# Optimization experiments

Hardware: AMD Instinct MI355X
Metric: run time of the kernel (lower is better)

The kernel has to match this reference:

```python
import jax, jax.numpy as jnp
import numpy as np

N_NODES = 50000
N_EDGES = 800000
NUM_FEATURES = 128
HIDDEN = 128
EMBED = 64
OUT_DIM = 1


def setup_inputs() -> dict:
    key = jax.random.key(0)
    ks = jax.random.split(key, 12)
    x = jax.random.normal(ks[0], (N_NODES, NUM_FEATURES), dtype=jnp.float32)
    edge_index = jax.random.randint(ks[1], (2, N_EDGES), 0, N_NODES, dtype=jnp.int64)

    def glorot(k, fan_in, fan_out):
        s = jnp.sqrt(6.0 / (fan_in + fan_out)).astype(jnp.float32)
        return jax.random.uniform(k, (fan_in, fan_out), jnp.float32, -s, s)

    return {
        "x": x,
        "edge_index": edge_index,
        "W1": glorot(ks[2], NUM_FEATURES, HIDDEN),
        "b1": jnp.zeros((HIDDEN,), jnp.float32),
        "Wh": glorot(ks[3], HIDDEN, HIDDEN),
        "bh": jnp.zeros((HIDDEN,), jnp.float32),
        "W2": glorot(ks[4], HIDDEN, EMBED),
        "b2": jnp.zeros((EMBED,), jnp.float32),
        "Wout": glorot(ks[5], EMBED, OUT_DIM),
        "bout": jnp.zeros((OUT_DIM,), jnp.float32),
    }


def _gcn_norm(edge_index, num_nodes):
    # Add self-loops, compute symmetric normalization deg^{-1/2} A_hat deg^{-1/2}
    loop = jnp.arange(num_nodes, dtype=edge_index.dtype)
    src = jnp.concatenate([edge_index[0], loop])
    dst = jnp.concatenate([edge_index[1], loop])
    deg = jax.ops.segment_sum(jnp.ones_like(dst, dtype=jnp.float32), dst,
                              num_segments=num_nodes)
    dis = jnp.where(deg > 0, jax.lax.rsqrt(jnp.maximum(deg, 1.0)), 0.0)
    norm = dis[src] * dis[dst]  # [E+N]
    return src, dst, norm


def _gcn_conv(h, W, b, src, dst, norm, num_nodes):
    h = h @ W  # linear transform first (PyG GCNConv)
    msg = h[src] * norm[:, None]  # gather + scale
    return jax.ops.segment_sum(msg, dst, num_segments=num_nodes) + b


def reference(x, edge_index, W1, b1, Wh, bh, W2, b2, Wout, bout):
    n = x.shape[0]
    src, dst, norm = _gcn_norm(edge_index, n)
    h = jax.nn.relu(_gcn_conv(x, W1, b1, src, dst, norm, n))  # dropout p=0 -> identity
    h = jax.nn.relu(_gcn_conv(h, Wh, bh, src, dst, norm, n))
    h = _gcn_conv(h, W2, b2, src, dst, norm, n)
    out = h @ Wout + bout
    return (out, h)
```

## Files before the change

kernel.cpp:

```cpp
#include <hip/hip_runtime.h>
#include <hip/hip_bf16.h>


#define N_NODES 50000
#define N_EDGES 800000
#define NBUCK 196
#define GB 196
#define EPB 4096

typedef __attribute__((ext_vector_type(8))) short short8;
typedef __attribute__((ext_vector_type(8))) unsigned short ushort8v;
typedef __attribute__((ext_vector_type(4))) float f32x4;

static __device__ __forceinline__ unsigned short f2bf(float f) {
    __hip_bfloat16 h = __float2bfloat16(f);
    return *reinterpret_cast<unsigned short*>(&h);
}
static __device__ __forceinline__ float bf2f(unsigned short u) {
    return __uint_as_float(((unsigned)u) << 16);
}

__global__ __launch_bounds__(256) void hist_wprep_kernel(
    const int* __restrict__ dstv, int* __restrict__ H, int nE, int* __restrict__ ticket,
    const float* __restrict__ W1, const float* __restrict__ Wh, const float* __restrict__ W2,
    unsigned short* __restrict__ W1hi, unsigned short* __restrict__ W1lo,
    unsigned short* __restrict__ Whhi, unsigned short* __restrict__ Whlo,
    unsigned short* __restrict__ W2hi, unsigned short* __restrict__ W2lo) {
    int gt = blockIdx.x * 256 + threadIdx.x;
    if (gt == 0) *ticket = 0;
    if (gt < 40960) {
        const float* W; unsigned short *Hi, *Lo; int nout, lt;
        if (gt < 16384)      { W = W1; Hi = W1hi; Lo = W1lo; nout = 128; lt = gt; }
        else if (gt < 32768) { W = Wh; Hi = Whhi; Lo = Whlo; nout = 128; lt = gt - 16384; }
        else                 { W = W2; Hi = W2hi; Lo = W2lo; nout = 64;  lt = gt - 32768; }
        int col = lt % nout, k = lt / nout;
        float v = W[lt];
        unsigned short hi = f2bf(v);
        unsigned short lo = f2bf(v - bf2f(hi));
        Hi[(size_t)col * 128 + k] = hi;
        Lo[(size_t)col * 128 + k] = lo;
    }

    __shared__ int h[NBUCK];
    for (int i = threadIdx.x; i < NBUCK; i += 256) h[i] = 0;
    __syncthreads();
    int base = blockIdx.x * EPB;
#pragma unroll
    for (int i = 0; i < EPB / 256; ++i) {
        int e = base + i * 256 + threadIdx.x;
        if (e < nE) atomicAdd(&h[dstv[e] >> 8], 1);
    }
    __syncthreads();
    for (int i = threadIdx.x; i < NBUCK; i += 256)
        H[i * GB + blockIdx.x] = h[i];
}

__global__ __launch_bounds__(256) void scan_kernel(int* __restrict__ H,
                                                   int* __restrict__ bsum,
                                                   int* __restrict__ bstart,
                                                   int* __restrict__ rowoff_last,
                                                   int* __restrict__ ticket) {
    __shared__ int s[256];
    __shared__ int lastFlag;
    int t = threadIdx.x, k = blockIdx.x;
    int v = (t < GB) ? H[k * GB + t] : 0;
    s[t] = v;
    __syncthreads();
    for (int off = 1; off < 256; off <<= 1) {
        int u = (t >= off) ? s[t - off] : 0;
        __syncthreads();
        s[t] += u;
        __syncthreads();
    }
    if (t < GB) H[k * GB + t] = s[t] - v;
    if (t == 255) {
        bsum[k] = s[255];
        __threadfence();
        int tk = atomicAdd(ticket, 1);
        lastFlag = (tk == NBUCK - 1);
    }
    __syncthreads();
    if (!lastFlag) return;
    __threadfence();
    int v2 = (t < NBUCK) ? bsum[t] : 0;
    s[t] = v2;
    __syncthreads();
    for (int off = 1; off < 256; off <<= 1) {
        int u = (t >= off) ? s[t - off] : 0;
        __syncthreads();
        s[t] += u;
        __syncthreads();
    }
    if (t < NBUCK) bstart[t] = s[t] - v2;
    if (t == 0) { bstart[NBUCK] = N_EDGES; *rowoff_last = N_EDGES; }
}

__global__ __launch_bounds__(256) void partition_kernel(const int* __restrict__ srcv,
                                                        const int* __restrict__ dstv,
                                                        const int* __restrict__ H,
                                                        const int* __restrict__ bstart,
                                                        unsigned int* __restrict__ P, int nE) {
    __shared__ int cur[NBUCK];
    for (int i = threadIdx.x; i < NBUCK; i += 256)
        cur[i] = bstart[i] + H[i * GB + blockIdx.x];
    __syncthreads();
    int base = blockIdx.x * EPB;
#pragma unroll
    for (int i = 0; i < EPB / 256; ++i) {
        int e = base + i * 256 + threadIdx.x;
        if (e < nE) {
            int d = dstv[e];
            unsigned int pk = (unsigned int)srcv[e] | ((unsigned int)(d & 255) << 16);
            int pos = atomicAdd(&cur[d >> 8], 1);
            P[pos] = pk;
        }
    }
}

__global__ __launch_bounds__(256) void bucket_csr_kernel(const unsigned int* __restrict__ P,
                                                         const int* __restrict__ bstart,
                                                         int* __restrict__ rowoff,
                                                         float* __restrict__ dis,
                                                         unsigned short* __restrict__ csr_src, int n) {
    __shared__ int cnt[256];
    __shared__ int s[256];
    __shared__ int cur[256];
    int t = threadIdx.x, k = blockIdx.x;
    int ebeg = bstart[k], eend = bstart[k + 1];
    cnt[t] = 0;
    __syncthreads();
    for (int e = ebeg + t; e < eend; e += 256)
        atomicAdd(&cnt[(P[e] >> 16) & 255], 1);
    __syncthreads();
    int myc = cnt[t];
    s[t] = myc;
    __syncthreads();
    for (int off = 1; off < 256; off <<= 1) {
        int v = (t >= off) ? s[t - off] : 0;
        __syncthreads();
        s[t] += v;
        __syncthreads();
    }
    int excl = s[t] - myc;
    int node = (k << 8) + t;
    if (node < n) {
        rowoff[node] = ebeg + excl;
        dis[node] = rsqrtf((float)(myc + 1));
    }
    cur[t] = ebeg + excl;
    __syncthreads();
    for (int e = ebeg + t; e < eend; e += 256) {
        unsigned int p = P[e];
        int pos = atomicAdd(&cur[(p >> 16) & 255], 1);
        csr_src[pos] = (unsigned short)(p & 0xFFFFu);
    }
}

template <int NOUT, bool SPLITA>
__global__ __launch_bounds__(256) void gemm_mfma_kernel(
    const float* __restrict__ A,
    const unsigned short* __restrict__ Ahi, const unsigned short* __restrict__ Alo,
    const unsigned short* __restrict__ Wthi, const unsigned short* __restrict__ Wtlo,
    const float* __restrict__ scale, unsigned short* __restrict__ C, int M) {
    constexpr int LDK = 136;
    __shared__ unsigned short sAhi[64 * LDK];
    __shared__ unsigned short sAlo[64 * LDK];

    int tid = threadIdx.x;
    int w = tid >> 6, lane = tid & 63;
    int quad = lane >> 4, m = lane & 15;
    int Rbase = blockIdx.x * 64, Cbase = blockIdx.y * 64;
    int r0 = (w & 1) * 32, c0 = (w >> 1) * 32;

    short8 bh[4][2], bl[4][2];
#pragma unroll
    for (int ks = 0; ks < 4; ++ks)
#pragma unroll
        for (int g = 0; g < 2; ++g) {
            size_t off = (size_t)(Cbase + c0 + g * 16 + m) * 128 + ks * 32 + quad * 8;
            bh[ks][g] = *(const short8*)(Wthi + off);
            bl[ks][g] = *(const short8*)(Wtlo + off);
        }

    if constexpr (SPLITA) {
        for (int i = tid; i < 64 * 16; i += 256) {
            int r = i >> 4, c8 = i & 15;
            int row = Rbase + r;
            short8 hv = {0,0,0,0,0,0,0,0}, lv = {0,0,0,0,0,0,0,0};
            if (row < M) {
                hv = *(const short8*)(Ahi + (size_t)row * 128 + c8 * 8);
                lv = *(const short8*)(Alo + (size_t)row * 128 + c8 * 8);
            }
            *(short8*)(sAhi + r * LDK + c8 * 8) = hv;
            *(short8*)(sAlo + r * LDK + c8 * 8) = lv;
        }
    } else {
        for (int i = tid; i < 64 * 32; i += 256) {
            int r = i >> 5, c4 = i & 31;
            int row = Rbase + r;
            float4 v = make_float4(0.f, 0.f, 0.f, 0.f);
            if (row < M) v = ((const float4*)(A + (size_t)row * 128))[c4];
            ushort4 hi, lo;
            hi.x = f2bf(v.x); lo.x = f2bf(v.x - bf2f(hi.x));
            hi.y = f2bf(v.y); lo.y = f2bf(v.y - bf2f(hi.y));
            hi.z = f2bf(v.z); lo.z = f2bf(v.z - bf2f(hi.z));
            hi.w = f2bf(v.w); lo.w = f2bf(v.w - bf2f(hi.w));
            *(ushort4*)(sAhi + r * LDK + c4 * 4) = hi;
            *(ushort4*)(sAlo + r * LDK + c4 * 4) = lo;
        }
    }
    __syncthreads();

    f32x4 z = {0.f, 0.f, 0.f, 0.f};
    f32x4 acc00 = z, acc01 = z, acc10 = z, acc11 = z;

#pragma unroll
    for (int ks = 0; ks < 4; ++ks) {
        int kof = ks * 32 + quad * 8;
        short8 ah0 = *(const short8*)(sAhi + (r0 + m) * LDK + kof);
        short8 ah1 = *(const short8*)(sAhi + (r0 + 16 + m) * LDK + kof);
        short8 al0 = *(const short8*)(sAlo + (r0 + m) * LDK + kof);
        short8 al1 = *(const short8*)(sAlo + (r0 + 16 + m) * LDK + kof);
        acc00 = __builtin_amdgcn_mfma_f32_16x16x32_bf16(ah0, bh[ks][0], acc00, 0, 0, 0);
        acc01 = __builtin_amdgcn_mfma_f32_16x16x32_bf16(ah0, bh[ks][1], acc01, 0, 0, 0);
        acc10 = __builtin_amdgcn_mfma_f32_16x16x32_bf16(ah1, bh[ks][0], acc10, 0, 0, 0);
        acc11 = __builtin_amdgcn_mfma_f32_16x16x32_bf16(ah1, bh[ks][1], acc11, 0, 0, 0);
        acc00 = __builtin_amdgcn_mfma_f32_16x16x32_bf16(ah0, bl[ks][0], acc00, 0, 0, 0);
        acc01 = __builtin_amdgcn_mfma_f32_16x16x32_bf16(ah0, bl[ks][1], acc01, 0, 0, 0);
        acc10 = __builtin_amdgcn_mfma_f32_16x16x32_bf16(ah1, bl[ks][0], acc10, 0, 0, 0);
        acc11 = __builtin_amdgcn_mfma_f32_16x16x32_bf16(ah1, bl[ks][1], acc11, 0, 0, 0);
        acc00 = __builtin_amdgcn_mfma_f32_16x16x32_bf16(al0, bh[ks][0], acc00, 0, 0, 0);
        acc01 = __builtin_amdgcn_mfma_f32_16x16x32_bf16(al0, bh[ks][1], acc01, 0, 0, 0);
        acc10 = __builtin_amdgcn_mfma_f32_16x16x32_bf16(al1, bh[ks][0], acc10, 0, 0, 0);
        acc11 = __builtin_amdgcn_mfma_f32_16x16x32_bf16(al1, bh[ks][1], acc11, 0, 0, 0);
    }

#pragma unroll
    for (int reg = 0; reg < 4; ++reg) {
        int row0g = Rbase + r0 + quad * 4 + reg;
        if (row0g < M) {
            float sc = scale[row0g];
            C[(size_t)row0g * NOUT + Cbase + c0 + m]      = f2bf(acc00[reg] * sc);
            C[(size_t)row0g * NOUT + Cbase + c0 + 16 + m] = f2bf(acc01[reg] * sc);
        }
        int row1g = row0g + 16;
        if (row1g < M) {
            float sc = scale[row1g];
            C[(size_t)row1g * NOUT + Cbase + c0 + m]      = f2bf(acc10[reg] * sc);
            C[(size_t)row1g * NOUT + Cbase + c0 + 16 + m] = f2bf(acc11[reg] * sc);
        }
    }
}

__global__ __launch_bounds__(256) void aggregate128_kernel(
    const int* __restrict__ rowoff, const unsigned short* __restrict__ csr_src,
    const float* __restrict__ dis, const unsigned short* __restrict__ tp,
    const float* __restrict__ bias,
    unsigned short* __restrict__ outHi, unsigned short* __restrict__ outLo, int n) {
    int gt = blockIdx.x * 256 + threadIdx.x;
    int node = gt >> 4;
    if (node >= n) return;
    int lc = gt & 15;

    float a[8] = {0.f,0.f,0.f,0.f,0.f,0.f,0.f,0.f};

#define ROW128(nd) (*(const ushort8v*)(tp + (size_t)(nd) * 128 + lc * 8))
#define ACC(u) { a[0] += bf2f(u[0]); a[1] += bf2f(u[1]); a[2] += bf2f(u[2]); a[3] += bf2f(u[3]); \
                 a[4] += bf2f(u[4]); a[5] += bf2f(u[5]); a[6] += bf2f(u[6]); a[7] += bf2f(u[7]); }

    { ushort8v u = ROW128(node); ACC(u); }

    int i = rowoff[node], end = rowoff[node + 1];
    for (; i + 8 <= end; i += 8) {
        int p0 = csr_src[i],     p1 = csr_src[i + 1], p2 = csr_src[i + 2], p3 = csr_src[i + 3];
        int p4 = csr_src[i + 4], p5 = csr_src[i + 5], p6 = csr_src[i + 6], p7 = csr_src[i + 7];
        ushort8v u0 = ROW128(p0), u1 = ROW128(p1), u2 = ROW128(p2), u3 = ROW128(p3);
        ushort8v u4 = ROW128(p4), u5 = ROW128(p5), u6 = ROW128(p6), u7 = ROW128(p7);
        ACC(u0); ACC(u1); ACC(u2); ACC(u3); ACC(u4); ACC(u5); ACC(u6); ACC(u7);
    }
    if (i + 4 <= end) {
        int p0 = csr_src[i], p1 = csr_src[i + 1], p2 = csr_src[i + 2], p3 = csr_src[i + 3];
        ushort8v u0 = ROW128(p0), u1 = ROW128(p1), u2 = ROW128(p2), u3 = ROW128(p3);
        ACC(u0); ACC(u1); ACC(u2); ACC(u3);
        i += 4;
    }
    if (i + 2 <= end) {
        int p0 = csr_src[i], p1 = csr_src[i + 1];
        ushort8v u0 = ROW128(p0), u1 = ROW128(p1);
        ACC(u0); ACC(u1);
        i += 2;
    }
    if (i < end) { ushort8v u = ROW128(csr_src[i]); ACC(u); }
#undef ROW128
#undef ACC

    float dd = dis[node];
    float4 b0 = ((const float4*)bias)[lc * 2];
    float4 b1 = ((const float4*)bias)[lc * 2 + 1];
    float r[8];
    r[0] = fmaxf(a[0] * dd + b0.x, 0.f);
    r[1] = fmaxf(a[1] * dd + b0.y, 0.f);
    r[2] = fmaxf(a[2] * dd + b0.z, 0.f);
    r[3] = fmaxf(a[3] * dd + b0.w, 0.f);
    r[4] = fmaxf(a[4] * dd + b1.x, 0.f);
    r[5] = fmaxf(a[5] * dd + b1.y, 0.f);
    r[6] = fmaxf(a[6] * dd + b1.z, 0.f);
    r[7] = fmaxf(a[7] * dd + b1.w, 0.f);
    ushort8v hi, lo;
#pragma unroll
    for (int j = 0; j < 8; ++j) {
        hi[j] = f2bf(r[j]);
        lo[j] = f2bf(r[j] - bf2f(hi[j]));
    }
    *(ushort8v*)(outHi + (size_t)node * 128 + lc * 8) = hi;
    *(ushort8v*)(outLo + (size_t)node * 128 + lc * 8) = lo;
}

__global__ __launch_bounds__(256) void aggregate64_head_kernel(
    const int* __restrict__ rowoff, const unsigned short* __restrict__ csr_src,
    const float* __restrict__ dis, const unsigned short* __restrict__ tp,
    const float* __restrict__ bias, const float* __restrict__ Wout,
    const float* __restrict__ bout, float* __restrict__ hout,
    float* __restrict__ out, int n) {
    int gt = blockIdx.x * 256 + threadIdx.x;
    int node = gt >> 4;
    if (node >= n) return;
    int lc = gt & 15;

    float a[4] = {0.f,0.f,0.f,0.f};

#define ROW64(nd) (*((const ushort4*)(tp + (size_t)(nd) * 64 + lc * 4)))
#define ACC2(u) { a[0] += bf2f(u.x); a[1] += bf2f(u.y); a[2] += bf2f(u.z); a[3] += bf2f(u.w); }

    { ushort4 u = ROW64(node); ACC2(u); }

    int i = rowoff[node], end = rowoff[node + 1];
    for (; i + 8 <= end; i += 8) {
        int p0 = csr_src[i],     p1 = csr_src[i + 1], p2 = csr_src[i + 2], p3 = csr_src[i + 3];
        int p4 = csr_src[i + 4], p5 = csr_src[i + 5], p6 = csr_src[i + 6], p7 = csr_src[i + 7];
        ushort4 u0 = ROW64(p0), u1 = ROW64(p1), u2 = ROW64(p2), u3 = ROW64(p3);
        ushort4 u4 = ROW64(p4), u5 = ROW64(p5), u6 = ROW64(p6), u7 = ROW64(p7);
        ACC2(u0); ACC2(u1); ACC2(u2); ACC2(u3); ACC2(u4); ACC2(u5); ACC2(u6); ACC2(u7);
    }
    if (i + 4 <= end) {
        int p0 = csr_src[i], p1 = csr_src[i + 1], p2 = csr_src[i + 2], p3 = csr_src[i + 3];
        ushort4 u0 = ROW64(p0), u1 = ROW64(p1), u2 = ROW64(p2), u3 = ROW64(p3);
        ACC2(u0); ACC2(u1); ACC2(u2); ACC2(u3);
        i += 4;
    }
    if (i + 2 <= end) {
        int p0 = csr_src[i], p1 = csr_src[i + 1];
        ushort4 u0 = ROW64(p0), u1 = ROW64(p1);
        ACC2(u0); ACC2(u1);
        i += 2;
    }
    if (i < end) { ushort4 u = ROW64(csr_src[i]); ACC2(u); }
#undef ROW64
#undef ACC2

    float dd = dis[node];
    float4 b = ((const float4*)bias)[lc];
    float4 hv;
    hv.x = a[0] * dd + b.x;
    hv.y = a[1] * dd + b.y;
    hv.z = a[2] * dd + b.z;
    hv.w = a[3] * dd + b.w;
    ((float4*)(hout + (size_t)node * 64))[lc] = hv;

    float4 wv = ((const float4*)Wout)[lc];
    float p = hv.x * wv.x + hv.y * wv.y + hv.z * wv.z + hv.w * wv.w;
#pragma unroll
    for (int off = 8; off > 0; off >>= 1) p += __shfl_xor(p, off);
    if (lc == 0) out[node] = p + bout[0];
}

extern "C" void kernel_launch(void* const* d_in, const int* in_sizes, int n_in,
                              void* d_out, int out_size, void* d_ws, size_t ws_size,
                              hipStream_t stream) {
    const float* x    = (const float*)d_in[0];
    const int*   ei   = (const int*)d_in[1];
    const float* W1   = (const float*)d_in[2];
    const float* b1   = (const float*)d_in[3];
    const float* Wh   = (const float*)d_in[4];
    const float* bh   = (const float*)d_in[5];
    const float* W2   = (const float*)d_in[6];
    const float* b2   = (const float*)d_in[7];
    const float* Wout = (const float*)d_in[8];
    const float* bout = (const float*)d_in[9];

    const int N = N_NODES;
    const int E = N_EDGES;
    const int* srcv = ei;
    const int* dstv = ei + E;

    float* out  = (float*)d_out;
    float* hout = (float*)d_out + N;

    char* ws = (char*)d_ws;
    auto alloc = [&](size_t bytes) -> char* {
        char* p = ws;
        ws += (bytes + 255) & ~(size_t)255;
        return p;
    };
    int*   H       = (int*)alloc(sizeof(int) * NBUCK * GB);
    int*   bsum    = (int*)alloc(sizeof(int) * NBUCK);
    int*   bstart  = (int*)alloc(sizeof(int) * (NBUCK + 1));
    int*   ticket  = (int*)alloc(sizeof(int) * 4);
    int*   rowoff  = (int*)alloc(sizeof(int) * (N + 1));
    unsigned int* P = (unsigned int*)alloc(sizeof(unsigned int) * E);
    unsigned short* csr_src = (unsigned short*)alloc(sizeof(unsigned short) * (E + 8));
    float* dis     = (float*)alloc(sizeof(float) * N);
    unsigned short* W1thi = (unsigned short*)alloc(sizeof(unsigned short) * 128 * 128);
    unsigned short* W1tlo = (unsigned short*)alloc(sizeof(unsigned short) * 128 * 128);
    unsigned short* Whthi = (unsigned short*)alloc(sizeof(unsigned short) * 128 * 128);
    unsigned short* Whtlo = (unsigned short*)alloc(sizeof(unsigned short) * 128 * 128);
    unsigned short* W2thi = (unsigned short*)alloc(sizeof(unsigned short) * 64 * 128);
    unsigned short* W2tlo = (unsigned short*)alloc(sizeof(unsigned short) * 64 * 128);
    unsigned short* bufT  = (unsigned short*)alloc(sizeof(unsigned short) * (size_t)N * 128);
    unsigned short* bufHi = (unsigned short*)alloc(sizeof(unsigned short) * (size_t)N * 128);
    unsigned short* bufLo = (unsigned short*)alloc(sizeof(unsigned short) * (size_t)N * 128);

    hist_wprep_kernel<<<GB, 256, 0, stream>>>(dstv, H, E, ticket,
                                              W1, Wh, W2, W1thi, W1tlo, Whthi, Whtlo, W2thi, W2tlo);
    scan_kernel<<<NBUCK, 256, 0, stream>>>(H, bsum, bstart, rowoff + N, ticket);
    partition_kernel<<<GB, 256, 0, stream>>>(srcv, dstv, H, bstart, P, E);
    bucket_csr_kernel<<<NBUCK, 256, 0, stream>>>(P, bstart, rowoff, dis, csr_src, N);

    const int aggBlocks = (N * 16 + 255) / 256;
    const int gemmRows = (N + 63) / 64;

    gemm_mfma_kernel<128, false><<<dim3(gemmRows, 2), 256, 0, stream>>>(
        x, nullptr, nullptr, W1thi, W1tlo, dis, bufT, N);
    aggregate128_kernel<<<aggBlocks, 256, 0, stream>>>(
        rowoff, csr_src, dis, bufT, b1, bufHi, bufLo, N);

    gemm_mfma_kernel<128, true><<<dim3(gemmRows, 2), 256, 0, stream>>>(
        nullptr, bufHi, bufLo, Whthi, Whtlo, dis, bufT, N);
    aggregate128_kernel<<<aggBlocks, 256, 0, stream>>>(
        rowoff, csr_src, dis, bufT, bh, bufHi, bufLo, N);

    gemm_mfma_kernel<64, true><<<dim3(gemmRows, 1), 256, 0, stream>>>(
        nullptr, bufHi, bufLo, W2thi, W2tlo, dis, bufT, N);
    aggregate64_head_kernel<<<aggBlocks, 256, 0, stream>>>(
        rowoff, csr_src, dis, bufT, b2, Wout, bout, hout, out, N);
}
```

Baseline: 258.9 us.

## Fuse aggregation with following GEMM via LDS tile and merge column blocks

```diff
diff --git a/kernel.cpp b/kernel.cpp
--- a/kernel.cpp
+++ b/kernel.cpp
@@ -156,164 +156,170 @@
     }
 }
 
-template <int NOUT, bool SPLITA>
-__global__ __launch_bounds__(256) void gemm_mfma_kernel(
+template <int NOUT>
+static __device__ __forceinline__ void gemm_from_lds(
+    const unsigned short* sAhi, const unsigned short* sAlo, int tid, int Rbase,
+    const unsigned short* __restrict__ Wthi, const unsigned short* __restrict__ Wtlo,
+    const float* __restrict__ scale, unsigned short* __restrict__ C, int M) {
+    constexpr int LDK = 136;
+    int w = tid >> 6, lane = tid & 63;
+    int quad = lane >> 4, m = lane & 15;
+    int r0 = (w & 1) * 32, c0 = (w >> 1) * 32;
+
+#pragma unroll
+    for (int cb = 0; cb < NOUT / 64; ++cb) {
+        int Cbase = cb * 64;
+        short8 bh[4][2], bl[4][2];
+#pragma unroll
+        for (int ks = 0; ks < 4; ++ks)
+#pragma unroll
+            for (int g = 0; g < 2; ++g) {
+                size_t off = (size_t)(Cbase + c0 + g * 16 + m) * 128 + ks * 32 + quad * 8;
+                bh[ks][g] = *(const short8*)(Wthi + off);
+                bl[ks][g] = *(const short8*)(Wtlo + off);
+            }
+
+        f32x4 z = {0.f, 0.f, 0.f, 0.f};
+        f32x4 acc00 = z, acc01 = z, acc10 = z, acc11 = z;
+#pragma unroll
+        for (int ks = 0; ks < 4; ++ks) {
+            int kof = ks * 32 + quad * 8;
+            short8 ah0 = *(const short8*)(sAhi + (r0 + m) * LDK + kof);
+            short8 ah1 = *(const short8*)(sAhi + (r0 + 16 + m) * LDK + kof);
+            short8 al0 = *(const short8*)(sAlo + (r0 + m) * LDK + kof);
+            short8 al1 = *(const short8*)(sAlo + (r0 + 16 + m) * LDK + kof);
+            acc00 = __builtin_amdgcn_mfma_f32_16x16x32_bf16(ah0, bh[ks][0], acc00, 0, 0, 0);
+            acc01 = __builtin_amdgcn_mfma_f32_16x16x32_bf16(ah0, bh[ks][1], acc01, 0, 0, 0);
+            acc10 = __builtin_amdgcn_mfma_f32_16x16x32_bf16(ah1, bh[ks][0], acc10, 0, 0, 0);
+            acc11 = __builtin_amdgcn_mfma_f32_16x16x32_bf16(ah1, bh[ks][1], acc11, 0, 0, 0);
+            acc00 = __builtin_amdgcn_mfma_f32_16x16x32_bf16(ah0, bl[ks][0], acc00, 0, 0, 0);
+            acc01 = __builtin_amdgcn_mfma_f32_16x16x32_bf16(ah0, bl[ks][1], acc01, 0, 0, 0);
+            acc10 = __builtin_amdgcn_mfma_f32_16x16x32_bf16(ah1, bl[ks][0], acc10, 0, 0, 0);
+            acc11 = __builtin_amdgcn_mfma_f32_16x16x32_bf16(ah1, bl[ks][1], acc11, 0, 0, 0);
+            acc00 = __builtin_amdgcn_mfma_f32_16x16x32_bf16(al0, bh[ks][0], acc00, 0, 0, 0);
+            acc01 = __builtin_amdgcn_mfma_f32_16x16x32_bf16(al0, bh[ks][1], acc01, 0, 0, 0);
+            acc10 = __builtin_amdgcn_mfma_f32_16x16x32_bf16(al1, bh[ks][0], acc10, 0, 0, 0);
+            acc11 = __builtin_amdgcn_mfma_f32_16x16x32_bf16(al1, bh[ks][1], acc11, 0, 0, 0);
+        }
+
+#pragma unroll
+        for (int reg = 0; reg < 4; ++reg) {
+            int row0g = Rbase + r0 + quad * 4 + reg;
+            if (row0g < M) {
+                float sc = scale[row0g];
+                C[(size_t)row0g * NOUT + Cbase + c0 + m]      = f2bf(acc00[reg] * sc);
+                C[(size_t)row0g * NOUT + Cbase + c0 + 16 + m] = f2bf(acc01[reg] * sc);
+            }
+            int row1g = row0g + 16;
+            if (row1g < M) {
+                float sc = scale[row1g];
+                C[(size_t)row1g * NOUT + Cbase + c0 + m]      = f2bf(acc10[reg] * sc);
+                C[(size_t)row1g * NOUT + Cbase + c0 + 16 + m] = f2bf(acc11[reg] * sc);
+            }
+        }
+    }
+}
+
+__global__ __launch_bounds__(256) void gemm1_kernel(
     const float* __restrict__ A,
-    const unsigned short* __restrict__ Ahi, const unsigned short* __restrict__ Alo,
     const unsigned short* __restrict__ Wthi, const unsigned short* __restrict__ Wtlo,
     const float* __restrict__ scale, unsigned short* __restrict__ C, int M) {
     constexpr int LDK = 136;
     __shared__ unsigned short sAhi[64 * LDK];
     __shared__ unsigned short sAlo[64 * LDK];
-
     int tid = threadIdx.x;
-    int w = tid >> 6, lane = tid & 63;
-    int quad = lane >> 4, m = lane & 15;
-    int Rbase = blockIdx.x * 64, Cbase = blockIdx.y * 64;
-    int r0 = (w & 1) * 32, c0 = (w >> 1) * 32;
-
-    short8 bh[4][2], bl[4][2];
-#pragma unroll
-    for (int ks = 0; ks < 4; ++ks)
-#pragma unroll
-        for (int g = 0; g < 2; ++g) {
-            size_t off = (size_t)(Cbase + c0 + g * 16 + m) * 128 + ks * 32 + quad * 8;
-            bh[ks][g] = *(const short8*)(Wthi + off);
-            bl[ks][g] = *(const short8*)(Wtlo + off);
-        }
-
-    if constexpr (SPLITA) {
-        for (int i = tid; i < 64 * 16; i += 256) {
-            int r = i >> 4, c8 = i & 15;
-            int row = Rbase + r;
-            short8 hv = {0,0,0,0,0,0,0,0}, lv = {0,0,0,0,0,0,0,0};
-            if (row < M) {
-                hv = *(const short8*)(Ahi + (size_t)row * 128 + c8 * 8);
-                lv = *(const short8*)(Alo + (size_t)row * 128 + c8 * 8);
-            }
-            *(short8*)(sAhi + r * LDK + c8 * 8) = hv;
-            *(short8*)(sAlo + r * LDK + c8 * 8) = lv;
-        }
-    } else {
-        for (int i = tid; i < 64 * 32; i += 256) {
-            int r = i >> 5, c4 = i & 31;
-            int row = Rbase + r;
-            float4 v = make_float4(0.f, 0.f, 0.f, 0.f);
-            if (row < M) v = ((const float4*)(A + (size_t)row * 128))[c4];
-            ushort4 hi, lo;
-            hi.x = f2bf(v.x); lo.x = f2bf(v.x - bf2f(hi.x));
-            hi.y = f2bf(v.y); lo.y = f2bf(v.y - bf2f(hi.y));
-            hi.z = f2bf(v.z); lo.z = f2bf(v.z - bf2f(hi.z));
-            hi.w = f2bf(v.w); lo.w = f2bf(v.w - bf2f(hi.w));
-            *(ushort4*)(sAhi + r * LDK + c4 * 4) = hi;
-            *(ushort4*)(sAlo + r * LDK + c4 * 4) = lo;
-        }
-    }
-    __syncthreads();
-
-    f32x4 z = {0.f, 0.f, 0.f, 0.f};
-    f32x4 acc00 = z, acc01 = z, acc10 = z, acc11 = z;
-
-#pragma unroll
-    for (int ks = 0; ks < 4; ++ks) {
-        int kof = ks * 32 + quad * 8;
-        short8 ah0 = *(const short8*)(sAhi + (r0 + m) * LDK + kof);
-        short8 ah1 = *(const short8*)(sAhi + (r0 + 16 + m) * LDK + kof);
-        short8 al0 = *(const short8*)(sAlo + (r0 + m) * LDK + kof);
-        short8 al1 = *(const short8*)(sAlo + (r0 + 16 + m) * LDK + kof);
-        acc00 = __builtin_amdgcn_mfma_f32_16x16x32_bf16(ah0, bh[ks][0], acc00, 0, 0, 0);
-        acc01 = __builtin_amdgcn_mfma_f32_16x16x32_bf16(ah0, bh[ks][1], acc01, 0, 0, 0);
-        acc10 = __builtin_amdgcn_mfma_f32_16x16x32_bf16(ah1, bh[ks][0], acc10, 0, 0, 0);
-        acc11 = __builtin_amdgcn_mfma_f32_16x16x32_bf16(ah1, bh[ks][1], acc11, 0, 0, 0);
-        acc00 = __builtin_amdgcn_mfma_f32_16x16x32_bf16(ah0, bl[ks][0], acc00, 0, 0, 0);
-        acc01 = __builtin_amdgcn_mfma_f32_16x16x32_bf16(ah0, bl[ks][1], acc01, 0, 0, 0);
-        acc10 = __builtin_amdgcn_mfma_f32_16x16x32_bf16(ah1, bl[ks][0], acc10, 0, 0, 0);
-        acc11 = __builtin_amdgcn_mfma_f32_16x16x32_bf16(ah1, bl[ks][1], acc11, 0, 0, 0);
-        acc00 = __builtin_amdgcn_mfma_f32_16x16x32_bf16(al0, bh[ks][0], acc00, 0, 0, 0);
-        acc01 = __builtin_amdgcn_mfma_f32_16x16x32_bf16(al0, bh[ks][1], acc01, 0, 0, 0);
-        acc10 = __builtin_amdgcn_mfma_f32_16x16x32_bf16(al1, bh[ks][0], acc10, 0, 0, 0);
-        acc11 = __builtin_amdgcn_mfma_f32_16x16x32_bf16(al1, bh[ks][1], acc11, 0, 0, 0);
-    }
-
-#pragma unroll
-    for (int reg = 0; reg < 4; ++reg) {
-        int row0g = Rbase + r0 + quad * 4 + reg;
-        if (row0g < M) {
-            float sc = scale[row0g];
-            C[(size_t)row0g * NOUT + Cbase + c0 + m]      = f2bf(acc00[reg] * sc);
-            C[(size_t)row0g * NOUT + Cbase + c0 + 16 + m] = f2bf(acc01[reg] * sc);
-        }
-        int row1g = row0g + 16;
-        if (row1g < M) {
-            float sc = scale[row1g];
-            C[(size_t)row1g * NOUT + Cbase + c0 + m]      = f2bf(acc10[reg] * sc);
-            C[(size_t)row1g * NOUT + Cbase + c0 + 16 + m] = f2bf(acc11[reg] * sc);
-        }
-    }
-}
-
-__global__ __launch_bounds__(256) void aggregate128_kernel(
+    int Rbase = blockIdx.x * 64;
+
+    for (int i = tid; i < 64 * 32; i += 256) {
+        int r = i >> 5, c4 = i & 31;
+        int row = Rbase + r;
+        float4 v = make_float4(0.f, 0.f, 0.f, 0.f);
+        if (row < M) v = ((const float4*)(A + (size_t)row * 128))[c4];
+        ushort4 hi, lo;
+        hi.x = f2bf(v.x); lo.x = f2bf(v.x - bf2f(hi.x));
+        hi.y = f2bf(v.y); lo.y = f2bf(v.y - bf2f(hi.y));
+        hi.z = f2bf(v.z); lo.z = f2bf(v.z - bf2f(hi.z));
+        hi.w = f2bf(v.w); lo.w = f2bf(v.w - bf2f(hi.w));
+        *(ushort4*)(sAhi + r * LDK + c4 * 4) = hi;
+        *(ushort4*)(sAlo + r * LDK + c4 * 4) = lo;
+    }
+    __syncthreads();
+    gemm_from_lds<128>(sAhi, sAlo, tid, Rbase, Wthi, Wtlo, scale, C, M);
+}
+
+template <int NOUT>
+__global__ __launch_bounds__(256) void agg_gemm_kernel(
     const int* __restrict__ rowoff, const unsigned short* __restrict__ csr_src,
     const float* __restrict__ dis, const unsigned short* __restrict__ tp,
     const float* __restrict__ bias,
-    unsigned short* __restrict__ outHi, unsigned short* __restrict__ outLo, int n) {
-    int gt = blockIdx.x * 256 + threadIdx.x;
-    int node = gt >> 4;
-    if (node >= n) return;
-    int lc = gt & 15;
-
-    float a[8] = {0.f,0.f,0.f,0.f,0.f,0.f,0.f,0.f};
-
+    const unsigned short* __restrict__ Wthi, const unsigned short* __restrict__ Wtlo,
+    unsigned short* __restrict__ C, int M) {
+    constexpr int LDK = 136;
+    __shared__ unsigned short sAhi[64 * LDK];
+    __shared__ unsigned short sAlo[64 * LDK];
+    int tid = threadIdx.x;
+    int Rbase = blockIdx.x * 64;
+    int s = tid >> 4, lc = tid & 15;
+
+    float4 b0 = ((const float4*)bias)[lc * 2];
+    float4 b1 = ((const float4*)bias)[lc * 2 + 1];
+
+#pragma unroll
+    for (int p = 0; p < 4; ++p) {
+        int r = p * 16 + s;
+        int node = Rbase + r;
+        ushort8v hi = {0,0,0,0,0,0,0,0}, lo = {0,0,0,0,0,0,0,0};
+        if (node < M) {
+            float a[8] = {0.f,0.f,0.f,0.f,0.f,0.f,0.f,0.f};
 #define ROW128(nd) (*(const ushort8v*)(tp + (size_t)(nd) * 128 + lc * 8))
 #define ACC(u) { a[0] += bf2f(u[0]); a[1] += bf2f(u[1]); a[2] += bf2f(u[2]); a[3] += bf2f(u[3]); \
                  a[4] += bf2f(u[4]); a[5] += bf2f(u[5]); a[6] += bf2f(u[6]); a[7] += bf2f(u[7]); }
-
-    { ushort8v u = ROW128(node); ACC(u); }
-
-    int i = rowoff[node], end = rowoff[node + 1];
-    for (; i + 8 <= end; i += 8) {
-        int p0 = csr_src[i],     p1 = csr_src[i + 1], p2 = csr_src[i + 2], p3 = csr_src[i + 3];
-        int p4 = csr_src[i + 4], p5 = csr_src[i + 5], p6 = csr_src[i + 6], p7 = csr_src[i + 7];
-        ushort8v u0 = ROW128(p0), u1 = ROW128(p1), u2 = ROW128(p2), u3 = ROW128(p3);
-        ushort8v u4 = ROW128(p4), u5 = ROW128(p5), u6 = ROW128(p6), u7 = ROW128(p7);
-        ACC(u0); ACC(u1); ACC(u2); ACC(u3); ACC(u4); ACC(u5); ACC(u6); ACC(u7);
-    }
-    if (i + 4 <= end) {
-        int p0 = csr_src[i], p1 = csr_src[i + 1], p2 = csr_src[i + 2], p3 = csr_src[i + 3];
-        ushort8v u0 = ROW128(p0), u1 = ROW128(p1), u2 = ROW128(p2), u3 = ROW128(p3);
-        ACC(u0); ACC(u1); ACC(u2); ACC(u3);
-        i += 4;
-    }
-    if (i + 2 <= end) {
-        int p0 = csr_src[i], p1 = csr_src[i + 1];
-        ushort8v u0 = ROW128(p0), u1 = ROW128(p1);
-        ACC(u0); ACC(u1);
-        i += 2;
-    }
-    if (i < end) { ushort8v u = ROW128(csr_src[i]); ACC(u); }
+            { ushort8v u = ROW128(node); ACC(u); }
+            int i = rowoff[node], end = rowoff[node + 1];
+            for (; i + 8 <= end; i += 8) {
+                int p0 = csr_src[i],     p1 = csr_src[i + 1], p2 = csr_src[i + 2], p3 = csr_src[i + 3];
+                int p4 = csr_src[i + 4], p5 = csr_src[i + 5], p6 = csr_src[i + 6], p7 = csr_src[i + 7];
+                ushort8v u0 = ROW128(p0), u1 = ROW128(p1), u2 = ROW128(p2), u3 = ROW128(p3);
+                ushort8v u4 = ROW128(p4), u5 = ROW128(p5), u6 = ROW128(p6), u7 = ROW128(p7);
+                ACC(u0); ACC(u1); ACC(u2); ACC(u3); ACC(u4); ACC(u5); ACC(u6); ACC(u7);
+            }
+            if (i + 4 <= end) {
+                int p0 = csr_src[i], p1 = csr_src[i + 1], p2 = csr_src[i + 2], p3 = csr_src[i + 3];
+                ushort8v u0 = ROW128(p0), u1 = ROW128(p1), u2 = ROW128(p2), u3 = ROW128(p3);
+                ACC(u0); ACC(u1); ACC(u2); ACC(u3);
+                i += 4;
+            }
+            if (i + 2 <= end) {
+                int p0 = csr_src[i], p1 = csr_src[i + 1];
+                ushort8v u0 = ROW128(p0), u1 = ROW128(p1);
+                ACC(u0); ACC(u1);
+                i += 2;
+            }
+            if (i < end) { ushort8v u = ROW128(csr_src[i]); ACC(u); }
 #undef ROW128
 #undef ACC
-
-    float dd = dis[node];
-    float4 b0 = ((const float4*)bias)[lc * 2];
-    float4 b1 = ((const float4*)bias)[lc * 2 + 1];
-    float r[8];
-    r[0] = fmaxf(a[0] * dd + b0.x, 0.f);
-    r[1] = fmaxf(a[1] * dd + b0.y, 0.f);
-    r[2] = fmaxf(a[2] * dd + b0.z, 0.f);
-    r[3] = fmaxf(a[3] * dd + b0.w, 0.f);
-    r[4] = fmaxf(a[4] * dd + b1.x, 0.f);
-    r[5] = fmaxf(a[5] * dd + b1.y, 0.f);
-    r[6] = fmaxf(a[6] * dd + b1.z, 0.f);
-    r[7] = fmaxf(a[7] * dd + b1.w, 0.f);
-    ushort8v hi, lo;
-#pragma unroll
-    for (int j = 0; j < 8; ++j) {
-        hi[j] = f2bf(r[j]);
-        lo[j] = f2bf(r[j] - bf2f(hi[j]));
-    }
-    *(ushort8v*)(outHi + (size_t)node * 128 + lc * 8) = hi;
-    *(ushort8v*)(outLo + (size_t)node * 128 + lc * 8) = lo;
+            float dd = dis[node];
+            float rr[8];
+            rr[0] = fmaxf(a[0] * dd + b0.x, 0.f);
+            rr[1] = fmaxf(a[1] * dd + b0.y, 0.f);
+            rr[2] = fmaxf(a[2] * dd + b0.z, 0.f);
+            rr[3] = fmaxf(a[3] * dd + b0.w, 0.f);
+            rr[4] = fmaxf(a[4] * dd + b1.x, 0.f);
+            rr[5] = fmaxf(a[5] * dd + b1.y, 0.f);
+            rr[6] = fmaxf(a[6] * dd + b1.z, 0.f);
+            rr[7] = fmaxf(a[7] * dd + b1.w, 0.f);
+#pragma unroll
+            for (int j = 0; j < 8; ++j) {
+                hi[j] = f2bf(rr[j]);
+                lo[j] = f2bf(rr[j] - bf2f(hi[j]));
+            }
+        }
+        *(ushort8v*)(sAhi + r * LDK + lc * 8) = hi;
+        *(ushort8v*)(sAlo + r * LDK + lc * 8) = lo;
+    }
+    __syncthreads();
+
+    gemm_from_lds<NOUT>(sAhi, sAlo, tid, Rbase, Wthi, Wtlo, dis, C, M);
 }
 
 __global__ __launch_bounds__(256) void aggregate64_head_kernel(
@@ -416,9 +422,8 @@
     unsigned short* Whtlo = (unsigned short*)alloc(sizeof(unsigned short) * 128 * 128);
     unsigned short* W2thi = (unsigned short*)alloc(sizeof(unsigned short) * 64 * 128);
     unsigned short* W2tlo = (unsigned short*)alloc(sizeof(unsigned short) * 64 * 128);
-    unsigned short* bufT  = (unsigned short*)alloc(sizeof(unsigned short) * (size_t)N * 128);
-    unsigned short* bufHi = (unsigned short*)alloc(sizeof(unsigned short) * (size_t)N * 128);
-    unsigned short* bufLo = (unsigned short*)alloc(sizeof(unsigned short) * (size_t)N * 128);
+    unsigned short* bufA  = (unsigned short*)alloc(sizeof(unsigned short) * (size_t)N * 128);
+    unsigned short* bufB  = (unsigned short*)alloc(sizeof(unsigned short) * (size_t)N * 128);
 
     hist_wprep_kernel<<<GB, 256, 0, stream>>>(dstv, H, E, ticket,
                                               W1, Wh, W2, W1thi, W1tlo, Whthi, Whtlo, W2thi, W2tlo);
@@ -426,21 +431,17 @@
     partition_kernel<<<GB, 256, 0, stream>>>(srcv, dstv, H, bstart, P, E);
     bucket_csr_kernel<<<NBUCK, 256, 0, stream>>>(P, bstart, rowoff, dis, csr_src, N);
 
-    const int aggBlocks = (N * 16 + 255) / 256;
-    const int gemmRows = (N + 63) / 64;
-
-    gemm_mfma_kernel<128, false><<<dim3(gemmRows, 2), 256, 0, stream>>>(
-        x, nullptr, nullptr, W1thi, W1tlo, dis, bufT, N);
-    aggregate128_kernel<<<aggBlocks, 256, 0, stream>>>(
-        rowoff, csr_src, dis, bufT, b1, bufHi, bufLo, N);
-
-    gemm_mfma_kernel<128, true><<<dim3(gemmRows, 2), 256, 0, stream>>>(
-        nullptr, bufHi, bufLo, Whthi, Whtlo, dis, bufT, N);
-    aggregate128_kernel<<<aggBlocks, 256, 0, stream>>>(
-        rowoff, csr_src, dis, bufT, bh, bufHi, bufLo, N);
-
-    gemm_mfma_kernel<64, true><<<dim3(gemmRows, 1), 256, 0, stream>>>(
-        nullptr, bufHi, bufLo, W2thi, W2tlo, dis, bufT, N);
+    const int aggBlocks  = (N * 16 + 255) / 256;
+    const int tileBlocks = (N + 63) / 64;
+
+    gemm1_kernel<<<tileBlocks, 256, 0, stream>>>(x, W1thi, W1tlo, dis, bufA, N);
+
+    agg_gemm_kernel<128><<<tileBlocks, 256, 0, stream>>>(
+        rowoff, csr_src, dis, bufA, b1, Whthi, Whtlo, bufB, N);
+
+    agg_gemm_kernel<64><<<tileBlocks, 256, 0, stream>>>(
+        rowoff, csr_src, dis, bufB, bh, W2thi, W2tlo, bufA, N);
+
     aggregate64_head_kernel<<<aggBlocks, 256, 0, stream>>>(
-        rowoff, csr_src, dis, bufT, b2, Wout, bout, hout, out, N);
-}
+        rowoff, csr_src, dis, bufA, b2, Wout, bout, hout, out, N);
+}
```

Result: slower. 265.9 us (+2.7%).
